# Kernel optimization log

Measured on AMD Instinct MI355X. Metric: run time of the kernel, lower is better.

The kernel has to match this reference:

```python
import jax, jax.numpy as jnp
import numpy as np
import math

D_MODEL = 1024
NHEAD = 16
HEAD_DIM = D_MODEL // NHEAD
SCALE = math.sqrt(HEAD_DIM)
B, TQ, TK = 8, 1024, 1024


def setup_inputs() -> dict:
    key = jax.random.key(0)
    ks = jax.random.split(key, 8)
    init = 0.02
    return {
        "query": jax.random.normal(ks[0], (B, TQ, D_MODEL), jnp.float32),
        "memory": jax.random.normal(ks[1], (B, TK, D_MODEL), jnp.float32),
        "coverage": jax.random.uniform(ks[2], (B, TK), jnp.float32),
        "Wq": jax.random.normal(ks[3], (D_MODEL, D_MODEL), jnp.float32) * init,
        "bq": jnp.zeros((D_MODEL,), jnp.float32),
        "Wk": jax.random.normal(ks[4], (D_MODEL, D_MODEL), jnp.float32) * init,
        "bk": jnp.zeros((D_MODEL,), jnp.float32),
        "Wv": jax.random.normal(ks[5], (D_MODEL, D_MODEL), jnp.float32) * init,
        "bv": jnp.zeros((D_MODEL,), jnp.float32),
        "Wo": jax.random.normal(ks[6], (D_MODEL, D_MODEL), jnp.float32) * init,
        "bo": jnp.zeros((D_MODEL,), jnp.float32),
        "Wcov": jax.random.normal(ks[7], (NHEAD, 1), jnp.float32) * init,
    }


def reference(query, memory, coverage, Wq, bq, Wk, bk, Wv, bv, Wo, bo, Wcov):
    b, tq, _ = query.shape
    tk = memory.shape[1]
    # projections, split into heads: [B, H, T, hd]
    Q = (query @ Wq.T + bq).reshape(b, tq, NHEAD, HEAD_DIM).transpose(0, 2, 1, 3)
    K = (memory @ Wk.T + bk).reshape(b, tk, NHEAD, HEAD_DIM).transpose(0, 2, 1, 3)
    V = (memory @ Wv.T + bv).reshape(b, tk, NHEAD, HEAD_DIM).transpose(0, 2, 1, 3)
    scores = jnp.einsum('bhqd,bhkd->bhqk', Q, K) / SCALE
    # coverage_proj: Linear(1, nhead, bias=False) -> outer product coverage x Wcov[:,0]
    cov_bias = jnp.einsum('bk,h->bhk', coverage, Wcov[:, 0])[:, :, None, :]  # [B,H,1,Tk]
    scores = scores + cov_bias
    attn = jax.nn.softmax(scores, axis=-1)
    # dropout is identity in eval/deterministic mode
    out = jnp.einsum('bhqk,bhkd->bhqd', attn, V).transpose(0, 2, 1, 3).reshape(b, tq, D_MODEL)
    out = out @ Wo.T + bo
    new_coverage = coverage + attn.mean(axis=1).sum(axis=1)  # [B,Tk]
    return out, new_coverage
```

## Files before the change

### kernel.cpp

```cpp
#include <hip/hip_runtime.h>

typedef __bf16 bf16_t;
typedef bf16_t bf16x8 __attribute__((ext_vector_type(8)));
typedef float f32x4 __attribute__((ext_vector_type(4)));

#define MFMA16(a, b, c) __builtin_amdgcn_mfma_f32_16x16x32_bf16(a, b, c, 0, 0, 0)

#define LOG2E 1.44269504f
#define C1 0.18033688f
#define EXP2(x) __builtin_amdgcn_exp2f(x)

#define WAIT_VM4_LGKM0 0x074
#define WAIT_VM2_LGKM0 0x072
#define WAIT_VM0_LGKM0 0x070

__device__ inline void barrier_ws() {
  __asm__ volatile("" ::: "memory");
  __builtin_amdgcn_s_barrier();
  __asm__ volatile("" ::: "memory");
}

__device__ inline void async_copy16(const bf16_t* g, bf16_t* l) {
  __builtin_amdgcn_global_load_lds(
      (const __attribute__((address_space(1))) void*)g,
      (__attribute__((address_space(3))) void*)l, 16, 0, 0);
}

__device__ inline bf16x8 lds_frag(const bf16_t* lds, int row, int c8) {
  return *(const bf16x8*)(lds + row * 64 + ((c8 ^ (row & 7)) << 3));
}

template <int NCHUNK, int NT>
__device__ inline void stage_tile(const bf16_t* __restrict__ g, size_t ld,
                                  bf16_t* lds, int tid) {
#pragma unroll
  for (int it = 0; it < NCHUNK / NT; ++it) {
    int f = it * NT + tid;
    int row = f >> 3;
    int c8 = (f & 7) ^ (row & 7);
    async_copy16(g + (size_t)row * ld + c8 * 8, lds + f * 8);
  }
}

__global__ __launch_bounds__(256) void convert_kernel(
    const float* __restrict__ q, const float* __restrict__ mem,
    const float* __restrict__ wq, const float* __restrict__ wk,
    const float* __restrict__ wv, const float* __restrict__ wo,
    const float* __restrict__ coverage, const float* __restrict__ Wcov,
    bf16_t* Xq, bf16_t* Xm, bf16_t* Wqb, bf16_t* Wkb, bf16_t* Wvb,
    bf16_t* Wob, float* covout, bf16_t* covE) {
  size_t i = ((size_t)blockIdx.x * 256 + threadIdx.x) * 8;
  if (i >= 20979712u) {
    size_t off = i - 20979712u;
    int k = (int)(off & 1023);
    int bh = (int)(off >> 10);
    int b = bh >> 4, h = bh & 15;
    float w = Wcov[h] * LOG2E;
    float4 c0 = *(const float4*)(coverage + (b << 10) + k);
    float4 c1 = *(const float4*)(coverage + (b << 10) + k + 4);
    union { bf16_t h8[8]; uint4 u; } t;
    t.h8[0] = (bf16_t)EXP2(c0.x * w); t.h8[1] = (bf16_t)EXP2(c0.y * w);
    t.h8[2] = (bf16_t)EXP2(c0.z * w); t.h8[3] = (bf16_t)EXP2(c0.w * w);
    t.h8[4] = (bf16_t)EXP2(c1.x * w); t.h8[5] = (bf16_t)EXP2(c1.y * w);
    t.h8[6] = (bf16_t)EXP2(c1.z * w); t.h8[7] = (bf16_t)EXP2(c1.w * w);
    *(uint4*)(covE + off) = t.u;
    return;
  }
  if (i >= 20971520u) {
    size_t off = i - 20971520u;
    *(float4*)(covout + off) = *(const float4*)(coverage + off);
    *(float4*)(covout + off + 4) = *(const float4*)(coverage + off + 4);
    return;
  }
  const float* src;
  bf16_t* dst;
  size_t off;
  if (i < 8388608u)        { src = q;   dst = Xq;  off = i; }
  else if (i < 16777216u)  { src = mem; dst = Xm;  off = i - 8388608u; }
  else if (i < 17825792u)  { src = wq;  dst = Wqb; off = i - 16777216u; }
  else if (i < 18874368u)  { src = wk;  dst = Wkb; off = i - 17825792u; }
  else if (i < 19922944u)  { src = wv;  dst = Wvb; off = i - 18874368u; }
  else                     { src = wo;  dst = Wob; off = i - 19922944u; }
  float4 f0 = *(const float4*)(src + off);
  float4 f1 = *(const float4*)(src + off + 4);
  union { bf16_t h[8]; uint4 u; } t;
  t.h[0] = (bf16_t)f0.x; t.h[1] = (bf16_t)f0.y;
  t.h[2] = (bf16_t)f0.z; t.h[3] = (bf16_t)f0.w;
  t.h[4] = (bf16_t)f1.x; t.h[5] = (bf16_t)f1.y;
  t.h[6] = (bf16_t)f1.z; t.h[7] = (bf16_t)f1.w;
  *(uint4*)(dst + off) = t.u;
}

__global__ __launch_bounds__(256) void gemm_qkv(
    const bf16_t* __restrict__ Xq, const bf16_t* __restrict__ Xm,
    const bf16_t* __restrict__ Wqkv, const float* __restrict__ bq,
    const float* __restrict__ bk, const float* __restrict__ bv,
    const bf16_t* __restrict__ covE, bf16_t* __restrict__ Qp,
    bf16_t* __restrict__ Kp, bf16_t* __restrict__ Vt) {
  __shared__ bf16_t As[128 * 64];
  __shared__ bf16_t Bs[128 * 64];
  const int tid = threadIdx.x;
  const int wave = tid >> 6, lane = tid & 63, quad = lane >> 4, c = lane & 15;
  const int wm = (wave & 1) * 64, wn = (wave >> 1) * 64;
  const size_t bm = blockIdx.x, bn = blockIdx.y;
  const int which = (int)(bn >> 3);
  const bf16_t* A = which ? Xm : Xq;
  const float* bias = which == 0 ? bq : (which == 1 ? bk : bv);
  const bf16_t* Ab = A + bm * 128 * 1024;
  const bf16_t* Bb = Wqkv + bn * 128 * 1024;
  const f32x4 z4 = {0.f, 0.f, 0.f, 0.f};
  f32x4 acc[4][4];
#pragma unroll
  for (int i = 0; i < 4; ++i)
#pragma unroll
    for (int j = 0; j < 4; ++j) acc[i][j] = z4;

  for (int kt = 0; kt < 16; ++kt) {
    if (kt) __syncthreads();
    stage_tile<1024, 256>(Ab + kt * 64, 1024, As, tid);
    stage_tile<1024, 256>(Bb + kt * 64, 1024, Bs, tid);
    __syncthreads();
#pragma unroll
    for (int ks = 0; ks < 2; ++ks) {
      bf16x8 af[4], bfr[4];
#pragma unroll
      for (int i = 0; i < 4; ++i)
        af[i] = lds_frag(As, wm + 16 * i + c, ks * 4 + quad);
#pragma unroll
      for (int j = 0; j < 4; ++j)
        bfr[j] = lds_frag(Bs, wn + 16 * j + c, ks * 4 + quad);
#pragma unroll
      for (int i = 0; i < 4; ++i)
#pragma unroll
        for (int j = 0; j < 4; ++j)
          acc[i][j] = MFMA16(af[i], bfr[j], acc[i][j]);
    }
  }
#pragma unroll
  for (int i = 0; i < 4; ++i)
#pragma unroll
    for (int j = 0; j < 4; ++j) {
      int gc = (int)bn * 128 + wn + 16 * j + c;
      int gcl = gc & 1023;
      float bvv = bias[gcl];
      if (which == 2) {
        int b = (int)(bm >> 3);
        int hh = gcl >> 6;
        int kk = (int)(bm & 7) * 128 + wm + 16 * i + quad * 4;
        union { bf16_t h4[4]; uint2 u; } ev;
        ev.u = *(const uint2*)(covE + ((size_t)(b * 16 + hh)) * 1024 + kk);
        union { bf16_t h4[4]; uint2 u; } pk;
#pragma unroll
        for (int r = 0; r < 4; ++r)
          pk.h4[r] = (bf16_t)((acc[i][j][r] + bvv) * (float)ev.h4[r]);
        *(uint2*)(Vt + ((size_t)(b * 1024 + gcl)) * 1024 + kk) = pk.u;
      } else {
        bf16_t* Cout = which ? Kp : Qp;
        float scale = which ? 1.0f : C1;
        int gr0 = (int)bm * 128 + wm + 16 * i + quad * 4;
#pragma unroll
        for (int r = 0; r < 4; ++r)
          Cout[(size_t)(gr0 + r) * 1024 + gcl] =
              (bf16_t)((acc[i][j][r] + bvv) * scale);
      }
    }
}

__global__ __launch_bounds__(256) void gemm_out(
    const bf16_t* __restrict__ A, const bf16_t* __restrict__ Bw,
    const float* __restrict__ bias, float* __restrict__ Cout) {
  __shared__ bf16_t As[128 * 64];
  __shared__ bf16_t Bs[128 * 64];
  const int tid = threadIdx.x;
  const int wave = tid >> 6, lane = tid & 63, quad = lane >> 4, c = lane & 15;
  const int wm = (wave & 1) * 64, wn = (wave >> 1) * 64;
  const size_t bm = blockIdx.x, bn = blockIdx.y;
  const bf16_t* Ab = A + bm * 128 * 1024;
  const bf16_t* Bb = Bw + bn * 128 * 1024;
  const f32x4 z4 = {0.f, 0.f, 0.f, 0.f};
  f32x4 acc[4][4];
#pragma unroll
  for (int i = 0; i < 4; ++i)
#pragma unroll
    for (int j = 0; j < 4; ++j) acc[i][j] = z4;

  for (int kt = 0; kt < 16; ++kt) {
    if (kt) __syncthreads();
    stage_tile<1024, 256>(Ab + kt * 64, 1024, As, tid);
    stage_tile<1024, 256>(Bb + kt * 64, 1024, Bs, tid);
    __syncthreads();
#pragma unroll
    for (int ks = 0; ks < 2; ++ks) {
      bf16x8 af[4], bfr[4];
#pragma unroll
      for (int i = 0; i < 4; ++i)
        af[i] = lds_frag(As, wm + 16 * i + c, ks * 4 + quad);
#pragma unroll
      for (int j = 0; j < 4; ++j)
        bfr[j] = lds_frag(Bs, wn + 16 * j + c, ks * 4 + quad);
#pragma unroll
      for (int i = 0; i < 4; ++i)
#pragma unroll
        for (int j = 0; j < 4; ++j)
          acc[i][j] = MFMA16(af[i], bfr[j], acc[i][j]);
    }
  }
#pragma unroll
  for (int i = 0; i < 4; ++i)
#pragma unroll
    for (int j = 0; j < 4; ++j) {
      int gc = (int)bn * 128 + wn + 16 * j + c;
      float bvv = bias[gc];
      int gr0 = (int)bm * 128 + wm + 16 * i + quad * 4;
#pragma unroll
      for (int r = 0; r < 4; ++r)
        Cout[(size_t)(gr0 + r) * 1024 + gc] = acc[i][j][r] + bvv;
    }
}

__global__ __launch_bounds__(256, 6) void attn_fwd(
    const bf16_t* __restrict__ Qp, const bf16_t* __restrict__ Kp,
    const bf16_t* __restrict__ Vt, const bf16_t* __restrict__ covE,
    bf16_t* __restrict__ Hb, float* __restrict__ linvG) {
  __shared__ bf16_t QPs[64 * 64];
  __shared__ bf16_t Ks[64 * 64];
  __shared__ bf16_t Vs[64 * 64];
  __shared__ bf16_t Es[1024];
  const int tid = threadIdx.x;
  const int wave = tid >> 6, lane = tid & 63, quad = lane >> 4, c = lane & 15;
  const int id = blockIdx.x;
  const int bh = id & 127, q0 = (id >> 7) * 64;
  const int b = bh >> 4, h = bh & 15;
  const f32x4 z4 = {0.f, 0.f, 0.f, 0.f};
  const bf16_t* Kbase = Kp + ((size_t)b * 1024) * 1024 + h * 64;
  const bf16_t* Vbase = Vt + ((size_t)(b * 1024 + h * 64)) * 1024;

  stage_tile<512, 256>(Qp + ((size_t)(b * 1024 + q0)) * 1024 + h * 64, 1024,
                       QPs, tid);
  if (tid < 128)
    async_copy16(covE + ((size_t)(b * 16 + h)) * 1024 + tid * 8,
                 Es + tid * 8);
  stage_tile<512, 256>(Kbase, 1024, Ks, tid);
  stage_tile<512, 256>(Vbase, 1024, Vs, tid);
  __builtin_amdgcn_s_waitcnt(WAIT_VM4_LGKM0);
  barrier_ws();
  bf16x8 qf0 = lds_frag(QPs, wave * 16 + c, quad);
  bf16x8 qf1 = lds_frag(QPs, wave * 16 + c, 4 + quad);
  bf16_t* Pw = &QPs[wave * 16 * 64];

  f32x4 O[4] = {z4, z4, z4, z4};
  f32x4 Ol = z4;

  for (int kt = 0; kt < 16; ++kt) {
    if (kt) {
      __syncthreads();
      stage_tile<512, 256>(Kbase + (size_t)kt * 64 * 1024, 1024, Ks, tid);
      stage_tile<512, 256>(Vbase + kt * 64, 1024, Vs, tid);
    }
    __syncthreads();
    f32x4 S[4] = {z4, z4, z4, z4};
#pragma unroll
    for (int j = 0; j < 4; ++j) {
      S[j] = MFMA16(lds_frag(Ks, j * 16 + c, quad), qf0, S[j]);
      S[j] = MFMA16(lds_frag(Ks, j * 16 + c, 4 + quad), qf1, S[j]);
    }
#pragma unroll
    for (int j = 0; j < 4; ++j) {
      union { bf16_t h4[4]; uint2 u; } pk;
#pragma unroll
      for (int r = 0; r < 4; ++r) pk.h4[r] = (bf16_t)EXP2(S[j][r]);
      int k8 = j * 2 + (quad >> 1);
      *(uint2*)(Pw + c * 64 + ((k8 ^ (c & 7)) << 3) + (quad & 1) * 4) = pk.u;
    }
#pragma unroll
    for (int ks = 0; ks < 2; ++ks) {
      bf16x8 pb =
          *(const bf16x8*)(Pw + c * 64 + (((ks * 4 + quad) ^ (c & 7)) << 3));
      bf16x8 ef = *(const bf16x8*)(Es + kt * 64 + ks * 32 + quad * 8);
#pragma unroll
      for (int j = 0; j < 4; ++j)
        O[j] = MFMA16(lds_frag(Vs, j * 16 + c, ks * 4 + quad), pb, O[j]);
      Ol = MFMA16(ef, pb, Ol);
    }
  }

  float linv = 1.f / Ol[0];
  if (quad == 0)
    linvG[((size_t)(b * 16 + h)) * 1024 + q0 + wave * 16 + c] = linv;

  size_t rowbase = ((size_t)(b * 1024 + q0 + wave * 16 + c)) * 1024 + h * 64;
#pragma unroll
  for (int j = 0; j < 4; ++j) {
    union { bf16_t h4[4]; uint2 u; } pk;
#pragma unroll
    for (int r = 0; r < 4; ++r) pk.h4[r] = (bf16_t)(O[j][r] * linv);
    *(uint2*)(Hb + rowbase + j * 16 + quad * 4) = pk.u;
  }
}

__global__ __launch_bounds__(256, 6) void cov_kernel(
    const bf16_t* __restrict__ Qp, const bf16_t* __restrict__ Kp,
    const bf16_t* __restrict__ covE, const float* __restrict__ linvG,
    float* __restrict__ covout) {
  __shared__ bf16_t Ks[64 * 64];
  __shared__ bf16_t Qs[2][64 * 64];
  __shared__ float covsum[64];
  const int tid = threadIdx.x;
  const int wave = tid >> 6, lane = tid & 63, quad = lane >> 4, c = lane & 15;
  const int id = blockIdx.x;
  const int bh = id & 127, k0 = (id >> 7) * 64;
  const int b = bh >> 4, h = bh & 15;
  const f32x4 z4 = {0.f, 0.f, 0.f, 0.f};
  const bf16_t* Qbase = Qp + ((size_t)b * 1024) * 1024 + h * 64;
  const float* lbase = linvG + ((size_t)(b * 16 + h)) * 1024 + wave * 16 + c;
  float lv_cur = lbase[0];

  if (tid < 64) covsum[tid] = 0.f;
  stage_tile<512, 256>(Kp + ((size_t)(b * 1024 + k0)) * 1024 + h * 64, 1024,
                       Ks, tid);
  stage_tile<512, 256>(Qbase, 1024, Qs[0], tid);

  float cs[4][4] = {};
  bf16x8 kf0[4], kf1[4];

  auto q_step = [&](int qt, const bf16_t* curQ, bf16_t* nxtQ) {
    float lv_nxt = 0.f;
    if (qt < 15) {
      lv_nxt = lbase[(qt + 1) * 64];
      stage_tile<512, 256>(Qbase + (size_t)(qt + 1) * 64 * 1024, 1024, nxtQ,
                           tid);
      __builtin_amdgcn_s_waitcnt(WAIT_VM2_LGKM0);
    } else {
      __builtin_amdgcn_s_waitcnt(WAIT_VM0_LGKM0);
    }
    barrier_ws();
    if (qt == 0) {
#pragma unroll
      for (int j = 0; j < 4; ++j) {
        kf0[j] = lds_frag(Ks, j * 16 + c, quad);
        kf1[j] = lds_frag(Ks, j * 16 + c, 4 + quad);
      }
    }
    bf16x8 qa = lds_frag(curQ, wave * 16 + c, quad);
    bf16x8 qb = lds_frag(curQ, wave * 16 + c, 4 + quad);
    f32x4 S[4] = {z4, z4, z4, z4};
#pragma unroll
    for (int j = 0; j < 4; ++j) {
      S[j] = MFMA16(kf0[j], qa, S[j]);
      S[j] = MFMA16(kf1[j], qb, S[j]);
    }
#pragma unroll
    for (int j = 0; j < 4; ++j)
#pragma unroll
      for (int r = 0; r < 4; ++r) cs[j][r] += EXP2(S[j][r]) * lv_cur;
    lv_cur = lv_nxt;
    barrier_ws();
  };

#pragma unroll 1
  for (int qt2 = 0; qt2 < 16; qt2 += 2) {
    q_step(qt2, Qs[0], Qs[1]);
    q_step(qt2 + 1, Qs[1], Qs[0]);
  }

#pragma unroll
  for (int j = 0; j < 4; ++j)
#pragma unroll
    for (int r = 0; r < 4; ++r) {
      float v = cs[j][r];
      v += __shfl_xor(v, 1);
      v += __shfl_xor(v, 2);
      v += __shfl_xor(v, 4);
      v += __shfl_xor(v, 8);
      if (c == 0) atomicAdd(&covsum[j * 16 + quad * 4 + r], v);
    }
  __syncthreads();
  if (tid < 64) {
    float e = (float)covE[((size_t)(b * 16 + h)) * 1024 + k0 + tid];
    atomicAdd(&covout[b * 1024 + k0 + tid], covsum[tid] * e * 0.0625f);
  }
}

extern "C" void kernel_launch(void* const* d_in, const int* in_sizes, int n_in,
                              void* d_out, int out_size, void* d_ws,
                              size_t ws_size, hipStream_t stream) {
  const float* query = (const float*)d_in[0];
  const float* memory = (const float*)d_in[1];
  const float* coverage = (const float*)d_in[2];
  const float* Wq = (const float*)d_in[3];
  const float* bq = (const float*)d_in[4];
  const float* Wk = (const float*)d_in[5];
  const float* bk = (const float*)d_in[6];
  const float* Wv = (const float*)d_in[7];
  const float* bv = (const float*)d_in[8];
  const float* Wo = (const float*)d_in[9];
  const float* bo = (const float*)d_in[10];
  const float* Wcov = (const float*)d_in[11];

  char* w = (char*)d_ws;
  const size_t MB = 1024 * 1024;
  bf16_t* Xq = (bf16_t*)(w + 0);
  bf16_t* Xm = (bf16_t*)(w + 16 * MB);
  bf16_t* Wqb = (bf16_t*)(w + 32 * MB);
  bf16_t* Wkb = (bf16_t*)(w + 34 * MB);
  bf16_t* Wvb = (bf16_t*)(w + 36 * MB);
  bf16_t* Wob = (bf16_t*)(w + 38 * MB);
  bf16_t* Qp = (bf16_t*)(w + 40 * MB);
  bf16_t* Kp = (bf16_t*)(w + 56 * MB);
  bf16_t* Vt = (bf16_t*)(w + 72 * MB);
  bf16_t* covE = (bf16_t*)(w + 88 * MB);
  bf16_t* Hb = (bf16_t*)(w + 0);
  float* linvG = (float*)(w + 16 * MB);

  float* out = (float*)d_out;
  float* covout = out + (size_t)8 * 1024 * 1024;

  convert_kernel<<<10308, 256, 0, stream>>>(query, memory, Wq, Wk, Wv, Wo,
                                            coverage, Wcov, Xq, Xm, Wqb, Wkb,
                                            Wvb, Wob, covout, covE);
  gemm_qkv<<<dim3(64, 24), 256, 0, stream>>>(Xq, Xm, Wqb, bq, bk, bv, covE,
                                             Qp, Kp, Vt);
  attn_fwd<<<2048, 256, 0, stream>>>(Qp, Kp, Vt, covE, Hb, linvG);
  cov_kernel<<<2048, 256, 0, stream>>>(Qp, Kp, covE, linvG, covout);
  gemm_out<<<dim3(64, 8), 256, 0, stream>>>(Hb, Wob, bo, out);
}
```

Measured before the change: 326.5 us.

## Enlarge attention blocks to 128 queries and merge coverage with output GEMM

The attention kernel now runs 512-thread blocks covering 128 query rows, so each K/V tile staged into LDS is shared by eight waves instead of four, halving K/V global traffic. The coverage kernel and the output projection GEMM are combined into one launch that dispatches on block index, removing a launch and letting the GEMM blocks overlap with the tail of the coverage work. In exchange, the larger attention blocks use more LDS and registers per block, which may lower occupancy, and the merged kernel's shared-memory size and register use are set by the larger of the two paths.

```diff
diff --git a/kernel.cpp b/kernel.cpp
--- a/kernel.cpp
+++ b/kernel.cpp
@@ -166,83 +166,31 @@
     }
 }
 
-__global__ __launch_bounds__(256) void gemm_out(
-    const bf16_t* __restrict__ A, const bf16_t* __restrict__ Bw,
-    const float* __restrict__ bias, float* __restrict__ Cout) {
-  __shared__ bf16_t As[128 * 64];
-  __shared__ bf16_t Bs[128 * 64];
-  const int tid = threadIdx.x;
-  const int wave = tid >> 6, lane = tid & 63, quad = lane >> 4, c = lane & 15;
-  const int wm = (wave & 1) * 64, wn = (wave >> 1) * 64;
-  const size_t bm = blockIdx.x, bn = blockIdx.y;
-  const bf16_t* Ab = A + bm * 128 * 1024;
-  const bf16_t* Bb = Bw + bn * 128 * 1024;
-  const f32x4 z4 = {0.f, 0.f, 0.f, 0.f};
-  f32x4 acc[4][4];
-#pragma unroll
-  for (int i = 0; i < 4; ++i)
-#pragma unroll
-    for (int j = 0; j < 4; ++j) acc[i][j] = z4;
-
-  for (int kt = 0; kt < 16; ++kt) {
-    if (kt) __syncthreads();
-    stage_tile<1024, 256>(Ab + kt * 64, 1024, As, tid);
-    stage_tile<1024, 256>(Bb + kt * 64, 1024, Bs, tid);
-    __syncthreads();
-#pragma unroll
-    for (int ks = 0; ks < 2; ++ks) {
-      bf16x8 af[4], bfr[4];
-#pragma unroll
-      for (int i = 0; i < 4; ++i)
-        af[i] = lds_frag(As, wm + 16 * i + c, ks * 4 + quad);
-#pragma unroll
-      for (int j = 0; j < 4; ++j)
-        bfr[j] = lds_frag(Bs, wn + 16 * j + c, ks * 4 + quad);
-#pragma unroll
-      for (int i = 0; i < 4; ++i)
-#pragma unroll
-        for (int j = 0; j < 4; ++j)
-          acc[i][j] = MFMA16(af[i], bfr[j], acc[i][j]);
-    }
-  }
-#pragma unroll
-  for (int i = 0; i < 4; ++i)
-#pragma unroll
-    for (int j = 0; j < 4; ++j) {
-      int gc = (int)bn * 128 + wn + 16 * j + c;
-      float bvv = bias[gc];
-      int gr0 = (int)bm * 128 + wm + 16 * i + quad * 4;
-#pragma unroll
-      for (int r = 0; r < 4; ++r)
-        Cout[(size_t)(gr0 + r) * 1024 + gc] = acc[i][j][r] + bvv;
-    }
-}
-
-__global__ __launch_bounds__(256, 6) void attn_fwd(
+__global__ __launch_bounds__(512, 8) void attn_fwd(
     const bf16_t* __restrict__ Qp, const bf16_t* __restrict__ Kp,
     const bf16_t* __restrict__ Vt, const bf16_t* __restrict__ covE,
     bf16_t* __restrict__ Hb, float* __restrict__ linvG) {
-  __shared__ bf16_t QPs[64 * 64];
+  __shared__ bf16_t QPs[128 * 64];
   __shared__ bf16_t Ks[64 * 64];
   __shared__ bf16_t Vs[64 * 64];
   __shared__ bf16_t Es[1024];
   const int tid = threadIdx.x;
   const int wave = tid >> 6, lane = tid & 63, quad = lane >> 4, c = lane & 15;
   const int id = blockIdx.x;
-  const int bh = id & 127, q0 = (id >> 7) * 64;
+  const int bh = id & 127, q0 = (id >> 7) * 128;
   const int b = bh >> 4, h = bh & 15;
   const f32x4 z4 = {0.f, 0.f, 0.f, 0.f};
   const bf16_t* Kbase = Kp + ((size_t)b * 1024) * 1024 + h * 64;
   const bf16_t* Vbase = Vt + ((size_t)(b * 1024 + h * 64)) * 1024;
 
-  stage_tile<512, 256>(Qp + ((size_t)(b * 1024 + q0)) * 1024 + h * 64, 1024,
-                       QPs, tid);
+  stage_tile<1024, 512>(Qp + ((size_t)(b * 1024 + q0)) * 1024 + h * 64, 1024,
+                        QPs, tid);
   if (tid < 128)
     async_copy16(covE + ((size_t)(b * 16 + h)) * 1024 + tid * 8,
                  Es + tid * 8);
-  stage_tile<512, 256>(Kbase, 1024, Ks, tid);
-  stage_tile<512, 256>(Vbase, 1024, Vs, tid);
-  __builtin_amdgcn_s_waitcnt(WAIT_VM4_LGKM0);
+  stage_tile<512, 512>(Kbase, 1024, Ks, tid);
+  stage_tile<512, 512>(Vbase, 1024, Vs, tid);
+  __builtin_amdgcn_s_waitcnt(WAIT_VM2_LGKM0);
   barrier_ws();
   bf16x8 qf0 = lds_frag(QPs, wave * 16 + c, quad);
   bf16x8 qf1 = lds_frag(QPs, wave * 16 + c, 4 + quad);
@@ -254,8 +202,8 @@
   for (int kt = 0; kt < 16; ++kt) {
     if (kt) {
       __syncthreads();
-      stage_tile<512, 256>(Kbase + (size_t)kt * 64 * 1024, 1024, Ks, tid);
-      stage_tile<512, 256>(Vbase + kt * 64, 1024, Vs, tid);
+      stage_tile<512, 512>(Kbase + (size_t)kt * 64 * 1024, 1024, Ks, tid);
+      stage_tile<512, 512>(Vbase + kt * 64, 1024, Vs, tid);
     }
     __syncthreads();
     f32x4 S[4] = {z4, z4, z4, z4};
@@ -298,16 +246,16 @@
   }
 }
 
-__global__ __launch_bounds__(256, 6) void cov_kernel(
-    const bf16_t* __restrict__ Qp, const bf16_t* __restrict__ Kp,
-    const bf16_t* __restrict__ covE, const float* __restrict__ linvG,
-    float* __restrict__ covout) {
-  __shared__ bf16_t Ks[64 * 64];
-  __shared__ bf16_t Qs[2][64 * 64];
-  __shared__ float covsum[64];
+__device__ __forceinline__ void cov_path(
+    char* smem, int id, const bf16_t* __restrict__ Qp,
+    const bf16_t* __restrict__ Kp, const bf16_t* __restrict__ covE,
+    const float* __restrict__ linvG, float* __restrict__ covout) {
+  bf16_t* Ks = (bf16_t*)smem;
+  bf16_t* Qs0 = (bf16_t*)(smem + 8192);
+  bf16_t* Qs1 = (bf16_t*)(smem + 16384);
+  float* covsum = (float*)(smem + 24576);
   const int tid = threadIdx.x;
   const int wave = tid >> 6, lane = tid & 63, quad = lane >> 4, c = lane & 15;
-  const int id = blockIdx.x;
   const int bh = id & 127, k0 = (id >> 7) * 64;
   const int b = bh >> 4, h = bh & 15;
   const f32x4 z4 = {0.f, 0.f, 0.f, 0.f};
@@ -318,7 +266,7 @@
   if (tid < 64) covsum[tid] = 0.f;
   stage_tile<512, 256>(Kp + ((size_t)(b * 1024 + k0)) * 1024 + h * 64, 1024,
                        Ks, tid);
-  stage_tile<512, 256>(Qbase, 1024, Qs[0], tid);
+  stage_tile<512, 256>(Qbase, 1024, Qs0, tid);
 
   float cs[4][4] = {};
   bf16x8 kf0[4], kf1[4];
@@ -359,8 +307,8 @@
 
 #pragma unroll 1
   for (int qt2 = 0; qt2 < 16; qt2 += 2) {
-    q_step(qt2, Qs[0], Qs[1]);
-    q_step(qt2 + 1, Qs[1], Qs[0]);
+    q_step(qt2, Qs0, Qs1);
+    q_step(qt2 + 1, Qs1, Qs0);
   }
 
 #pragma unroll
@@ -379,6 +327,72 @@
     float e = (float)covE[((size_t)(b * 16 + h)) * 1024 + k0 + tid];
     atomicAdd(&covout[b * 1024 + k0 + tid], covsum[tid] * e * 0.0625f);
   }
+}
+
+__device__ __forceinline__ void gemm_out_path(
+    char* smem, int id2, const bf16_t* __restrict__ A,
+    const bf16_t* __restrict__ Bw, const float* __restrict__ bias,
+    float* __restrict__ Cout) {
+  bf16_t* As = (bf16_t*)smem;
+  bf16_t* Bs = (bf16_t*)(smem + 16384);
+  const int tid = threadIdx.x;
+  const int wave = tid >> 6, lane = tid & 63, quad = lane >> 4, c = lane & 15;
+  const int wm = (wave & 1) * 64, wn = (wave >> 1) * 64;
+  const size_t bm = id2 & 63, bn = id2 >> 6;
+  const bf16_t* Ab = A + bm * 128 * 1024;
+  const bf16_t* Bb = Bw + bn * 128 * 1024;
+  const f32x4 z4 = {0.f, 0.f, 0.f, 0.f};
+  f32x4 acc[4][4];
+#pragma unroll
+  for (int i = 0; i < 4; ++i)
+#pragma unroll
+    for (int j = 0; j < 4; ++j) acc[i][j] = z4;
+
+  for (int kt = 0; kt < 16; ++kt) {
+    if (kt) __syncthreads();
+    stage_tile<1024, 256>(Ab + kt * 64, 1024, As, tid);
+    stage_tile<1024, 256>(Bb + kt * 64, 1024, Bs, tid);
+    __syncthreads();
+#pragma unroll
+    for (int ks = 0; ks < 2; ++ks) {
+      bf16x8 af[4], bfr[4];
+#pragma unroll
+      for (int i = 0; i < 4; ++i)
+        af[i] = lds_frag(As, wm + 16 * i + c, ks * 4 + quad);
+#pragma unroll
+      for (int j = 0; j < 4; ++j)
+        bfr[j] = lds_frag(Bs, wn + 16 * j + c, ks * 4 + quad);
+#pragma unroll
+      for (int i = 0; i < 4; ++i)
+#pragma unroll
+        for (int j = 0; j < 4; ++j)
+          acc[i][j] = MFMA16(af[i], bfr[j], acc[i][j]);
+    }
+  }
+#pragma unroll
+  for (int i = 0; i < 4; ++i)
+#pragma unroll
+    for (int j = 0; j < 4; ++j) {
+      int gc = (int)bn * 128 + wn + 16 * j + c;
+      float bvv = bias[gc];
+      int gr0 = (int)bm * 128 + wm + 16 * i + quad * 4;
+#pragma unroll
+      for (int r = 0; r < 4; ++r)
+        Cout[(size_t)(gr0 + r) * 1024 + gc] = acc[i][j][r] + bvv;
+    }
+}
+
+__global__ __launch_bounds__(256) void tail_kernel(
+    const bf16_t* __restrict__ Qp, const bf16_t* __restrict__ Kp,
+    const bf16_t* __restrict__ covE, const float* __restrict__ linvG,
+    float* __restrict__ covout, const bf16_t* __restrict__ Hb,
+    const bf16_t* __restrict__ Wob, const float* __restrict__ bo,
+    float* __restrict__ out) {
+  __shared__ __align__(16) char smem[33024];
+  if (blockIdx.x < 2048)
+    cov_path(smem, blockIdx.x, Qp, Kp, covE, linvG, covout);
+  else
+    gemm_out_path(smem, blockIdx.x - 2048, Hb, Wob, bo, out);
 }
 
 extern "C" void kernel_launch(void* const* d_in, const int* in_sizes, int n_in,
@@ -420,7 +434,7 @@
                                             Wvb, Wob, covout, covE);
   gemm_qkv<<<dim3(64, 24), 256, 0, stream>>>(Xq, Xm, Wqb, bq, bk, bv, covE,
                                              Qp, Kp, Vt);
-  attn_fwd<<<2048, 256, 0, stream>>>(Qp, Kp, Vt, covE, Hb, linvG);
-  cov_kernel<<<2048, 256, 0, stream>>>(Qp, Kp, covE, linvG, covout);
-  gemm_out<<<dim3(64, 8), 256, 0, stream>>>(Hb, Wob, bo, out);
-}
+  attn_fwd<<<1024, 512, 0, stream>>>(Qp, Kp, Vt, covE, Hb, linvG);
+  tail_kernel<<<2560, 256, 0, stream>>>(Qp, Kp, covE, linvG, covout, Hb, Wob,
+                                        bo, out);
+}
```

Result: faster. 297.0 us (-9.0%).
